# Kernel optimization log

Hardware: AMD Instinct MI355X
Metric: run time of the kernel (lower is better)

## Reference

```python
import jax, jax.numpy as jnp
import numpy as np

B, N, E = 128, 2048, 32768   # events, nodes per history graph, temporal edges per graph
C, TC, H = 4, 4, 2           # channels, time_channels, heads (hardcoded in source)
DH = C // H
L = 2                        # num_layers


def setup_inputs() -> dict:
    key = jax.random.key(0)
    ks = jax.random.split(key, 16)
    return {
        "x": jax.random.normal(ks[0], (B, N, C), jnp.float32),
        "edge_index": jax.random.randint(ks[1], (B, 2, E), 0, N),
        "edge_time": jax.random.uniform(ks[2], (B, E), jnp.float32),
        "timestamp": jax.random.uniform(ks[3], (B,), jnp.float32),
        "src_index": jax.random.randint(ks[4], (B,), 0, N),
        "dst_index": jax.random.randint(ks[5], (B,), 0, N),
        "time_w": jax.random.normal(ks[6], (TC,), jnp.float32),
        "time_b": jax.random.normal(ks[7], (TC,), jnp.float32),
        "Wq": jax.random.normal(ks[8], (L, C, C), jnp.float32) / np.sqrt(C).astype(np.float32),
        "Wk": jax.random.normal(ks[9], (L, C + TC, C), jnp.float32) / np.sqrt(C + TC).astype(np.float32),
        "Wv": jax.random.normal(ks[10], (L, C + TC, C), jnp.float32) / np.sqrt(C + TC).astype(np.float32),
        "Wo": jax.random.normal(ks[11], (L, C, C), jnp.float32) / np.sqrt(C).astype(np.float32),
        "bo": jnp.zeros((L, C), jnp.float32),
        "W_lin": jax.random.normal(ks[12], (2 * C + TC, 2), jnp.float32) / np.sqrt(2 * C + TC).astype(np.float32),
        "b_lin": jnp.zeros((2,), jnp.float32),
    }


def _time_enc(t, w, b):
    # TimeEncoder: cos(t * w + b)  (Bochner-style functional time encoding)
    return jnp.cos(t[..., None] * w + b)


def _encode(x, src, dst, phi, Wq, Wk, Wv, Wo, bo):
    # seg id per edge: (batch, dst node) -> flat segment for segment softmax
    seg = (jnp.arange(B, dtype=dst.dtype)[:, None] * N + dst).reshape(-1)  # [B*E]
    h = x
    for l in range(L):
        h_src = jnp.take_along_axis(h, src[:, :, None], axis=1)            # [B,E,C] gather source feats
        msg = jnp.concatenate([h_src, phi], axis=-1)                       # [B,E,C+TC]
        q = (h @ Wq[l]).reshape(B, N, C)                                   # [B,N,C]
        k = (msg @ Wk[l]).reshape(B, E, H, DH)
        v = (msg @ Wv[l]).reshape(B, E, H, DH)
        q_e = jnp.take_along_axis(q, dst[:, :, None], axis=1).reshape(B, E, H, DH)
        logits = (q_e * k).sum(-1) / np.float32(np.sqrt(DH))               # [B,E,H]
        lf = logits.reshape(B * E, H)
        m = jax.ops.segment_max(lf, seg, num_segments=B * N)               # stable softmax max
        p = jnp.exp(lf - m[seg])
        s = jax.ops.segment_sum(p, seg, num_segments=B * N)
        agg = jax.ops.segment_sum(p[:, :, None] * v.reshape(B * E, H, DH), seg, num_segments=B * N)
        attn = (agg / jnp.where(s == 0, 1.0, s)[:, :, None]).reshape(B, N, C)
        h = jax.nn.relu(h + attn @ Wo[l] + bo[l])                          # residual + out-proj + relu
    return h


def reference(x, edge_index, edge_time, timestamp, src_index, dst_index,
              time_w, time_b, Wq, Wk, Wv, Wo, bo, W_lin, b_lin):
    src, dst = edge_index[:, 0, :], edge_index[:, 1, :]
    dt = timestamp[:, None] - edge_time                                    # [B,E] time deltas vs query time
    phi = _time_enc(dt, time_w, time_b)                                    # [B,E,TC]
    h = _encode(x, src, dst, phi, Wq, Wk, Wv, Wo, bo)                      # [B,N,C]
    bidx = jnp.arange(B)
    src_x = h[bidx, src_index]                                             # [B,C]
    dst_x = h[bidx, dst_index]                                             # [B,C]
    time_x = _time_enc(timestamp, time_w, time_b)                          # [B,TC]
    feats = jnp.concatenate([src_x, dst_x, time_x], axis=-1)               # [B,12]
    return feats @ W_lin + b_lin                                           # [B,2]
```

## Files before the change

kernel.cpp:

```cpp
#include <hip/hip_runtime.h>

namespace {

constexpr int B = 128, N = 2048, E = 32768;
constexpr int LOG2N = 11, LOG2E = 15;
constexpr int QE = E / 4;
constexpr int LOG2QE = 13;

constexpr size_t OFF_H0 = 0;
constexpr size_t OFF_H1 = 4u * 1024 * 1024;
constexpr size_t OFF_S8 = 8u * 1024 * 1024;
constexpr size_t OFF_RP = 40u * 1024 * 1024;

__global__ __launch_bounds__(1024) void sort_kernel(const int* __restrict__ edge_index,
                                                    const float* __restrict__ edge_time,
                                                    const float* __restrict__ timestamp,
                                                    int2* __restrict__ sorted8,
                                                    int* __restrict__ row_ptr) {
  __shared__ int  cnt[N];
  __shared__ int  wsum[16];
  __shared__ int2 rec[QE];
  int blk = blockIdx.x, b = blk >> 2, q = blk & 3, t = threadIdx.x;

  cnt[t] = 0; cnt[t + 1024] = 0;
  __syncthreads();

  const int* src_arr = edge_index + (((size_t)(2 * b)) << LOG2E) + q * QE;
  const int* dst_arr = edge_index + (((size_t)(2 * b + 1)) << LOG2E) + q * QE;
  const float* et    = edge_time + (((size_t)b) << LOG2E) + q * QE;
  float ts = timestamp[b];

  for (int e = t; e < QE; e += 1024) atomicAdd(&cnt[dst_arr[e]], 1);
  __syncthreads();

  int i0 = 2 * t, i1 = 2 * t + 1;
  int l0 = cnt[i0], l1 = cnt[i1];
  int sum = l0 + l1;
  int lane = t & 63, wid = t >> 6;
  int incl = sum;
#pragma unroll
  for (int d = 1; d < 64; d <<= 1) {
    int v = __shfl_up(incl, d, 64);
    if (lane >= d) incl += v;
  }
  if (lane == 63) wsum[wid] = incl;
  __syncthreads();
  if (t < 16) {
    int v = wsum[t];
    int inc = v;
#pragma unroll
    for (int d = 1; d < 16; d <<= 1) {
      int u = __shfl_up(inc, d, 16);
      if (t >= d) inc += u;
    }
    wsum[t] = inc - v;
  }
  __syncthreads();
  int run = wsum[wid] + (incl - sum);
  int run2 = run + l0;
  int* rp = row_ptr + (size_t)blk * (N + 1);
  rp[i0] = run;
  rp[i1] = run2;
  if (t == 1023) rp[N] = QE;
  cnt[i0] = run;
  cnt[i1] = run2;
  __syncthreads();

  for (int e = t; e < QE; e += 1024) {
    int dst = dst_arr[e];
    int src = src_arr[e];
    float dt = ts - et[e];
    int pos = atomicAdd(&cnt[dst], 1);
    rec[pos] = make_int2(src, __float_as_int(dt));
  }
  __syncthreads();

  const int4* rec4 = (const int4*)rec;
  int4* out4 = (int4*)(sorted8 + (((size_t)blk) << LOG2QE));
#pragma unroll
  for (int i = t; i < QE / 2; i += 1024) out4[i] = rec4[i];
}

__global__ __launch_bounds__(1024) void layer_kernel(const float4* __restrict__ h_in,
                                                     float4* __restrict__ h_out,
                                                     const int* __restrict__ row_ptr,
                                                     const int2* __restrict__ sorted8,
                                                     const float* __restrict__ tw,
                                                     const float* __restrict__ tb,
                                                     const float* __restrict__ Wq,
                                                     const float* __restrict__ Wk,
                                                     const float* __restrict__ Wv,
                                                     const float* __restrict__ Wo,
                                                     const float* __restrict__ bo) {
  __shared__ float4 lh[N];
  int blk = blockIdx.x, b = blk >> 1, half = blk & 1, t = threadIdx.x;

  const float4* hb = h_in + (((size_t)b) << LOG2N);
  lh[t] = hb[t];
  lh[t + 1024] = hb[t + 1024];

  float twf[4], tbf[4], wq[16], wkh[16], wkp[16], wvh[16], wvp[16];
#pragma unroll
  for (int j = 0; j < 4; j++) { twf[j] = tw[j]; tbf[j] = tb[j]; }
#pragma unroll
  for (int j = 0; j < 16; j++) wq[j] = Wq[j];
#pragma unroll
  for (int j = 0; j < 16; j++) { wkh[j] = Wk[j]; wkp[j] = Wk[16 + j]; }
#pragma unroll
  for (int j = 0; j < 16; j++) { wvh[j] = Wv[j]; wvp[j] = Wv[16 + j]; }
  __syncthreads();

  int n = half * 1024 + t;
  float4 hn = lh[n];
  const float RS2 = 0.70710678118654752f;
  float q0 = (hn.x * wq[0] + hn.y * wq[4] + hn.z * wq[8]  + hn.w * wq[12]) * RS2;
  float q1 = (hn.x * wq[1] + hn.y * wq[5] + hn.z * wq[9]  + hn.w * wq[13]) * RS2;
  float q2 = (hn.x * wq[2] + hn.y * wq[6] + hn.z * wq[10] + hn.w * wq[14]) * RS2;
  float q3 = (hn.x * wq[3] + hn.y * wq[7] + hn.z * wq[11] + hn.w * wq[15]) * RS2;

  float wH0[4], wH1[4], wA[4], wB[4];
#pragma unroll
  for (int i = 0; i < 4; i++) {
    wH0[i] = q0 * wkh[i * 4 + 0] + q1 * wkh[i * 4 + 1];
    wH1[i] = q2 * wkh[i * 4 + 2] + q3 * wkh[i * 4 + 3];
    wA[i]  = q0 * wkp[i * 4 + 0] + q1 * wkp[i * 4 + 1];
    wB[i]  = q2 * wkp[i * 4 + 2] + q3 * wkp[i * 4 + 3];
  }

  int stage = 0;
  int addr, rem, total;
  int b1, b2, b3, c1, c2, c3;
  {
    const int* rp0 = row_ptr + (size_t)(b * 4 + 0) * (N + 1);
    const int* rp1 = row_ptr + (size_t)(b * 4 + 1) * (N + 1);
    const int* rp2 = row_ptr + (size_t)(b * 4 + 2) * (N + 1);
    const int* rp3 = row_ptr + (size_t)(b * 4 + 3) * (N + 1);
    int s0 = rp0[n], e0 = rp0[n + 1];
    int s1 = rp1[n], e1 = rp1[n + 1];
    int s2 = rp2[n], e2 = rp2[n + 1];
    int s3 = rp3[n], e3 = rp3[n + 1];
    int c0 = e0 - s0; c1 = e1 - s1; c2 = e2 - s2; c3 = e3 - s3;
    total = c0 + c1 + c2 + c3;
    addr = ((b * 4 + 0) << LOG2QE) + s0; rem = c0;
    b1 = ((b * 4 + 1) << LOG2QE) + s1;
    b2 = ((b * 4 + 2) << LOG2QE) + s2;
    b3 = ((b * 4 + 3) << LOG2QE) + s3;
  }
  while (rem == 0 && stage < 3) {
    ++stage;
    addr = (stage == 1) ? b1 : (stage == 2) ? b2 : b3;
    rem  = (stage == 1) ? c1 : (stage == 2) ? c2 : c3;
  }

  float m0 = -INFINITY, m1 = -INFINITY;
  float s0v = 0.f, s1v = 0.f, a00 = 0.f, a01 = 0.f, a10 = 0.f, a11 = 0.f;

  int2 rcCur = sorted8[addr];
  for (int it = 0; it < total; ++it) {
    int2 rc = rcCur;
    ++addr; --rem;
    while (rem == 0 && stage < 3) {
      ++stage;
      addr = (stage == 1) ? b1 : (stage == 2) ? b2 : b3;
      rem  = (stage == 1) ? c1 : (stage == 2) ? c2 : c3;
    }
    rcCur = sorted8[addr];

    float dt = __int_as_float(rc.y);
    float4 hs = lh[rc.x];
    float ph0 = __cosf(dt * twf[0] + tbf[0]);
    float ph1 = __cosf(dt * twf[1] + tbf[1]);
    float ph2 = __cosf(dt * twf[2] + tbf[2]);
    float ph3 = __cosf(dt * twf[3] + tbf[3]);

    float l0 = hs.x * wH0[0] + hs.y * wH0[1] + hs.z * wH0[2] + hs.w * wH0[3]
             + ph0 * wA[0] + ph1 * wA[1] + ph2 * wA[2] + ph3 * wA[3];
    float l1 = hs.x * wH1[0] + hs.y * wH1[1] + hs.z * wH1[2] + hs.w * wH1[3]
             + ph0 * wB[0] + ph1 * wB[1] + ph2 * wB[2] + ph3 * wB[3];

    float v0 = hs.x * wvh[0] + hs.y * wvh[4] + hs.z * wvh[8]  + hs.w * wvh[12]
             + ph0 * wvp[0] + ph1 * wvp[4] + ph2 * wvp[8]  + ph3 * wvp[12];
    float v1 = hs.x * wvh[1] + hs.y * wvh[5] + hs.z * wvh[9]  + hs.w * wvh[13]
             + ph0 * wvp[1] + ph1 * wvp[5] + ph2 * wvp[9]  + ph3 * wvp[13];
    float v2 = hs.x * wvh[2] + hs.y * wvh[6] + hs.z * wvh[10] + hs.w * wvh[14]
             + ph0 * wvp[2] + ph1 * wvp[6] + ph2 * wvp[10] + ph3 * wvp[14];
    float v3 = hs.x * wvh[3] + hs.y * wvh[7] + hs.z * wvh[11] + hs.w * wvh[15]
             + ph0 * wvp[3] + ph1 * wvp[7] + ph2 * wvp[11] + ph3 * wvp[15];

    float d0 = l0 - m0;
    float e0 = __expf(fminf(d0, -d0));
    bool  g0 = d0 > 0.f;
    float p0  = g0 ? 1.f : e0;
    float sc0 = g0 ? e0 : 1.f;
    m0 = fmaxf(m0, l0);
    s0v = s0v * sc0 + p0;
    a00 = a00 * sc0 + p0 * v0;
    a01 = a01 * sc0 + p0 * v1;
    float d1 = l1 - m1;
    float e1 = __expf(fminf(d1, -d1));
    bool  g1 = d1 > 0.f;
    float p1  = g1 ? 1.f : e1;
    float sc1 = g1 ? e1 : 1.f;
    m1 = fmaxf(m1, l1);
    s1v = s1v * sc1 + p1;
    a10 = a10 * sc1 + p1 * v2;
    a11 = a11 * sc1 + p1 * v3;
  }

  float den0 = (s0v == 0.f) ? 1.f : s0v;
  float den1 = (s1v == 0.f) ? 1.f : s1v;
  float at0 = a00 / den0, at1 = a01 / den0, at2 = a10 / den1, at3 = a11 / den1;

  float wof[16], bof[4];
#pragma unroll
  for (int j = 0; j < 16; j++) wof[j] = Wo[j];
#pragma unroll
  for (int j = 0; j < 4; j++) bof[j] = bo[j];

  float o0 = bof[0] + at0 * wof[0] + at1 * wof[4] + at2 * wof[8]  + at3 * wof[12];
  float o1 = bof[1] + at0 * wof[1] + at1 * wof[5] + at2 * wof[9]  + at3 * wof[13];
  float o2 = bof[2] + at0 * wof[2] + at1 * wof[6] + at2 * wof[10] + at3 * wof[14];
  float o3 = bof[3] + at0 * wof[3] + at1 * wof[7] + at2 * wof[11] + at3 * wof[15];
  h_out[(((size_t)b) << LOG2N) + n] =
      make_float4(fmaxf(hn.x + o0, 0.f), fmaxf(hn.y + o1, 0.f),
                  fmaxf(hn.z + o2, 0.f), fmaxf(hn.w + o3, 0.f));
}

__global__ void final_kernel(const float4* __restrict__ h,
                             const int* __restrict__ src_index, const int* __restrict__ dst_index,
                             const float* __restrict__ timestamp,
                             const float* __restrict__ tw,
                             const float* __restrict__ tb,
                             const float* __restrict__ W_lin,
                             const float* __restrict__ b_lin,
                             float* __restrict__ out) {
  int b = threadIdx.x;
  if (b >= B) return;
  float4 sx = h[(((size_t)b) << LOG2N) + src_index[b]];
  float4 dx = h[(((size_t)b) << LOG2N) + dst_index[b]];
  float ts = timestamp[b];
  float f[12];
  f[0] = sx.x; f[1] = sx.y; f[2] = sx.z; f[3] = sx.w;
  f[4] = dx.x; f[5] = dx.y; f[6] = dx.z; f[7] = dx.w;
#pragma unroll
  for (int j = 0; j < 4; j++) f[8 + j] = __cosf(ts * tw[j] + tb[j]);
#pragma unroll
  for (int c = 0; c < 2; c++) {
    float o = b_lin[c];
#pragma unroll
    for (int j = 0; j < 12; j++) o += f[j] * W_lin[j * 2 + c];
    out[b * 2 + c] = o;
  }
}

}

extern "C" void kernel_launch(void* const* d_in, const int* in_sizes, int n_in,
                              void* d_out, int out_size, void* d_ws, size_t ws_size,
                              hipStream_t stream) {
  (void)in_sizes; (void)n_in; (void)out_size; (void)ws_size;
  const float* x         = (const float*)d_in[0];
  const int*   edge_idx  = (const int*)d_in[1];
  const float* edge_time = (const float*)d_in[2];
  const float* timestamp = (const float*)d_in[3];
  const int*   src_index = (const int*)d_in[4];
  const int*   dst_index = (const int*)d_in[5];
  const float* time_w    = (const float*)d_in[6];
  const float* time_b    = (const float*)d_in[7];
  const float* Wq        = (const float*)d_in[8];
  const float* Wk        = (const float*)d_in[9];
  const float* Wv        = (const float*)d_in[10];
  const float* Wo        = (const float*)d_in[11];
  const float* bo        = (const float*)d_in[12];
  const float* W_lin     = (const float*)d_in[13];
  const float* b_lin     = (const float*)d_in[14];

  char* ws = (char*)d_ws;
  float4* h0      = (float4*)(ws + OFF_H0);
  float4* h1      = (float4*)(ws + OFF_H1);
  int2*   sorted8 = (int2*)(ws + OFF_S8);
  int*    row_ptr = (int*)(ws + OFF_RP);

  sort_kernel<<<4 * B, 1024, 0, stream>>>(edge_idx, edge_time, timestamp, sorted8, row_ptr);

  layer_kernel<<<2 * B, 1024, 0, stream>>>((const float4*)x, h1, row_ptr, sorted8,
                                           time_w, time_b,
                                           Wq + 0 * 16, Wk + 0 * 32, Wv + 0 * 32,
                                           Wo + 0 * 16, bo + 0 * 4);
  layer_kernel<<<2 * B, 1024, 0, stream>>>(h1, h0, row_ptr, sorted8,
                                           time_w, time_b,
                                           Wq + 1 * 16, Wk + 1 * 32, Wv + 1 * 32,
                                           Wo + 1 * 16, bo + 1 * 4);

  final_kernel<<<1, 128, 0, stream>>>(h0, src_index, dst_index, timestamp, time_w, time_b,
                                      W_lin, b_lin, (float*)d_out);
}
```

Before: 168.0 us.

## Drop online-softmax max tracking, use hardware cos/exp2, and process two edges per iteration

Removes the running-max rescaling from the per-node attention loop. Logits are pre-scaled by log2(e) so the loop can call v_exp_f32 directly, and each edge's weight simply adds into the sums. The time-encoding cos becomes a v_cos_f32 inline asm, with inputs pre-scaled by 1/(2π). The edge loop is unrolled by two with independent accumulators to break the serial dependency chain. Without max subtraction, exp can overflow for large logits, so correctness now depends on the logits staying small. The hardware cos may also lose accuracy for large arguments.

New measurement: 173.2 us. +3.1%, slower.

```diff
diff --git a/kernel.cpp b/kernel.cpp
--- a/kernel.cpp
+++ b/kernel.cpp
@@ -99,9 +99,11 @@
   lh[t] = hb[t];
   lh[t + 1024] = hb[t + 1024];
 
-  float twf[4], tbf[4], wq[16], wkh[16], wkp[16], wvh[16], wvp[16];
-#pragma unroll
-  for (int j = 0; j < 4; j++) { twf[j] = tw[j]; tbf[j] = tb[j]; }
+  constexpr float INV2PI = 0.15915494309189535f;
+  constexpr float QSCALE = 0.70710678118654752f * 1.4426950408889634f;
+  float twf2[4], tbf2[4], wq[16], wkh[16], wkp[16], wvh[16], wvp[16];
+#pragma unroll
+  for (int j = 0; j < 4; j++) { twf2[j] = tw[j] * INV2PI; tbf2[j] = tb[j] * INV2PI; }
 #pragma unroll
   for (int j = 0; j < 16; j++) wq[j] = Wq[j];
 #pragma unroll
@@ -111,24 +113,22 @@
   __syncthreads();
 
   int n = half * 1024 + t;
-  float4 hn = lh[n];
-  const float RS2 = 0.70710678118654752f;
-  float q0 = (hn.x * wq[0] + hn.y * wq[4] + hn.z * wq[8]  + hn.w * wq[12]) * RS2;
-  float q1 = (hn.x * wq[1] + hn.y * wq[5] + hn.z * wq[9]  + hn.w * wq[13]) * RS2;
-  float q2 = (hn.x * wq[2] + hn.y * wq[6] + hn.z * wq[10] + hn.w * wq[14]) * RS2;
-  float q3 = (hn.x * wq[3] + hn.y * wq[7] + hn.z * wq[11] + hn.w * wq[15]) * RS2;
-
-  float wH0[4], wH1[4], wA[4], wB[4];
-#pragma unroll
-  for (int i = 0; i < 4; i++) {
-    wH0[i] = q0 * wkh[i * 4 + 0] + q1 * wkh[i * 4 + 1];
-    wH1[i] = q2 * wkh[i * 4 + 2] + q3 * wkh[i * 4 + 3];
-    wA[i]  = q0 * wkp[i * 4 + 0] + q1 * wkp[i * 4 + 1];
-    wB[i]  = q2 * wkp[i * 4 + 2] + q3 * wkp[i * 4 + 3];
-  }
-
-  int stage = 0;
-  int addr, rem, total;
+  {
+    float4 hn = lh[n];
+    float q0 = (hn.x * wq[0] + hn.y * wq[4] + hn.z * wq[8]  + hn.w * wq[12]) * QSCALE;
+    float q1 = (hn.x * wq[1] + hn.y * wq[5] + hn.z * wq[9]  + hn.w * wq[13]) * QSCALE;
+    float q2 = (hn.x * wq[2] + hn.y * wq[6] + hn.z * wq[10] + hn.w * wq[14]) * QSCALE;
+    float q3 = (hn.x * wq[3] + hn.y * wq[7] + hn.z * wq[11] + hn.w * wq[15]) * QSCALE;
+#pragma unroll
+    for (int i = 0; i < 4; i++) {
+      wq[i]      = q0 * wkh[i * 4 + 0] + q1 * wkh[i * 4 + 1];
+      wq[4 + i]  = q2 * wkh[i * 4 + 2] + q3 * wkh[i * 4 + 3];
+      wq[8 + i]  = q0 * wkp[i * 4 + 0] + q1 * wkp[i * 4 + 1];
+      wq[12 + i] = q2 * wkp[i * 4 + 2] + q3 * wkp[i * 4 + 3];
+    }
+  }
+
+  int stage = 0, addr, rem, total;
   int b1, b2, b3, c1, c2, c3;
   {
     const int* rp0 = row_ptr + (size_t)(b * 4 + 0) * (N + 1);
@@ -145,67 +145,94 @@
     b1 = ((b * 4 + 1) << LOG2QE) + s1;
     b2 = ((b * 4 + 2) << LOG2QE) + s2;
     b3 = ((b * 4 + 3) << LOG2QE) + s3;
-  }
-  while (rem == 0 && stage < 3) {
-    ++stage;
-    addr = (stage == 1) ? b1 : (stage == 2) ? b2 : b3;
-    rem  = (stage == 1) ? c1 : (stage == 2) ? c2 : c3;
-  }
-
-  float m0 = -INFINITY, m1 = -INFINITY;
-  float s0v = 0.f, s1v = 0.f, a00 = 0.f, a01 = 0.f, a10 = 0.f, a11 = 0.f;
-
-  int2 rcCur = sorted8[addr];
-  for (int it = 0; it < total; ++it) {
-    int2 rc = rcCur;
-    ++addr; --rem;
-    while (rem == 0 && stage < 3) {
+    while (rem <= 0 && stage < 3) {
       ++stage;
       addr = (stage == 1) ? b1 : (stage == 2) ? b2 : b3;
       rem  = (stage == 1) ? c1 : (stage == 2) ? c2 : c3;
     }
-    rcCur = sorted8[addr];
-
-    float dt = __int_as_float(rc.y);
-    float4 hs = lh[rc.x];
-    float ph0 = __cosf(dt * twf[0] + tbf[0]);
-    float ph1 = __cosf(dt * twf[1] + tbf[1]);
-    float ph2 = __cosf(dt * twf[2] + tbf[2]);
-    float ph3 = __cosf(dt * twf[3] + tbf[3]);
-
-    float l0 = hs.x * wH0[0] + hs.y * wH0[1] + hs.z * wH0[2] + hs.w * wH0[3]
-             + ph0 * wA[0] + ph1 * wA[1] + ph2 * wA[2] + ph3 * wA[3];
-    float l1 = hs.x * wH1[0] + hs.y * wH1[1] + hs.z * wH1[2] + hs.w * wH1[3]
-             + ph0 * wB[0] + ph1 * wB[1] + ph2 * wB[2] + ph3 * wB[3];
-
-    float v0 = hs.x * wvh[0] + hs.y * wvh[4] + hs.z * wvh[8]  + hs.w * wvh[12]
-             + ph0 * wvp[0] + ph1 * wvp[4] + ph2 * wvp[8]  + ph3 * wvp[12];
-    float v1 = hs.x * wvh[1] + hs.y * wvh[5] + hs.z * wvh[9]  + hs.w * wvh[13]
-             + ph0 * wvp[1] + ph1 * wvp[5] + ph2 * wvp[9]  + ph3 * wvp[13];
-    float v2 = hs.x * wvh[2] + hs.y * wvh[6] + hs.z * wvh[10] + hs.w * wvh[14]
-             + ph0 * wvp[2] + ph1 * wvp[6] + ph2 * wvp[10] + ph3 * wvp[14];
-    float v3 = hs.x * wvh[3] + hs.y * wvh[7] + hs.z * wvh[11] + hs.w * wvh[15]
-             + ph0 * wvp[3] + ph1 * wvp[7] + ph2 * wvp[11] + ph3 * wvp[15];
-
-    float d0 = l0 - m0;
-    float e0 = __expf(fminf(d0, -d0));
-    bool  g0 = d0 > 0.f;
-    float p0  = g0 ? 1.f : e0;
-    float sc0 = g0 ? e0 : 1.f;
-    m0 = fmaxf(m0, l0);
-    s0v = s0v * sc0 + p0;
-    a00 = a00 * sc0 + p0 * v0;
-    a01 = a01 * sc0 + p0 * v1;
-    float d1 = l1 - m1;
-    float e1 = __expf(fminf(d1, -d1));
-    bool  g1 = d1 > 0.f;
-    float p1  = g1 ? 1.f : e1;
-    float sc1 = g1 ? e1 : 1.f;
-    m1 = fmaxf(m1, l1);
-    s1v = s1v * sc1 + p1;
-    a10 = a10 * sc1 + p1 * v2;
-    a11 = a11 * sc1 + p1 * v3;
-  }
+  }
+
+#define ADV() do { ++addr; --rem;                                   \
+    while (rem <= 0 && stage < 3) { ++stage;                        \
+      addr = (stage == 1) ? b1 : (stage == 2) ? b2 : b3;            \
+      rem  = (stage == 1) ? c1 : (stage == 2) ? c2 : c3; } } while (0)
+#define HW_COS(d, s) asm("v_cos_f32 %0, %1" : "=v"(d) : "v"(s))
+#define HW_EXP2(d, s) asm("v_exp_f32 %0, %1" : "=v"(d) : "v"(s))
+
+  float sA0 = 0.f, sA1 = 0.f, aA00 = 0.f, aA01 = 0.f, aA10 = 0.f, aA11 = 0.f;
+  float sB0 = 0.f, sB1 = 0.f, aB00 = 0.f, aB01 = 0.f, aB10 = 0.f, aB11 = 0.f;
+
+  int itc = (total + 1) >> 1;
+  int2 rA = sorted8[addr]; ADV();
+  int2 rB = sorted8[addr]; ADV();
+
+  for (int it = 0; it < itc; ++it) {
+    int2 cA = rA, cB = rB;
+    rA = sorted8[addr]; ADV();
+    rB = sorted8[addr]; ADV();
+
+    bool vB = (2 * it + 1) < total;
+    float dtA = __int_as_float(cA.y);
+    float dtB = vB ? __int_as_float(cB.y) : 0.f;
+    float4 hsA = lh[cA.x & (N - 1)];
+    float4 hsB = lh[cB.x & (N - 1)];
+
+    float phA0, phA1, phA2, phA3, phB0, phB1, phB2, phB3;
+    HW_COS(phA0, dtA * twf2[0] + tbf2[0]);
+    HW_COS(phA1, dtA * twf2[1] + tbf2[1]);
+    HW_COS(phA2, dtA * twf2[2] + tbf2[2]);
+    HW_COS(phA3, dtA * twf2[3] + tbf2[3]);
+    HW_COS(phB0, dtB * twf2[0] + tbf2[0]);
+    HW_COS(phB1, dtB * twf2[1] + tbf2[1]);
+    HW_COS(phB2, dtB * twf2[2] + tbf2[2]);
+    HW_COS(phB3, dtB * twf2[3] + tbf2[3]);
+
+    float lA0 = hsA.x * wq[0] + hsA.y * wq[1] + hsA.z * wq[2]  + hsA.w * wq[3]
+              + phA0 * wq[8] + phA1 * wq[9] + phA2 * wq[10] + phA3 * wq[11];
+    float lA1 = hsA.x * wq[4] + hsA.y * wq[5] + hsA.z * wq[6]  + hsA.w * wq[7]
+              + phA0 * wq[12] + phA1 * wq[13] + phA2 * wq[14] + phA3 * wq[15];
+    float lB0 = hsB.x * wq[0] + hsB.y * wq[1] + hsB.z * wq[2]  + hsB.w * wq[3]
+              + phB0 * wq[8] + phB1 * wq[9] + phB2 * wq[10] + phB3 * wq[11];
+    float lB1 = hsB.x * wq[4] + hsB.y * wq[5] + hsB.z * wq[6]  + hsB.w * wq[7]
+              + phB0 * wq[12] + phB1 * wq[13] + phB2 * wq[14] + phB3 * wq[15];
+
+    float pA0, pA1, eB0, eB1;
+    HW_EXP2(pA0, lA0);
+    HW_EXP2(pA1, lA1);
+    HW_EXP2(eB0, lB0);
+    HW_EXP2(eB1, lB1);
+    float pB0 = vB ? eB0 : 0.f;
+    float pB1 = vB ? eB1 : 0.f;
+
+    float vA0 = hsA.x * wvh[0] + hsA.y * wvh[4] + hsA.z * wvh[8]  + hsA.w * wvh[12]
+              + phA0 * wvp[0] + phA1 * wvp[4] + phA2 * wvp[8]  + phA3 * wvp[12];
+    float vA1 = hsA.x * wvh[1] + hsA.y * wvh[5] + hsA.z * wvh[9]  + hsA.w * wvh[13]
+              + phA0 * wvp[1] + phA1 * wvp[5] + phA2 * wvp[9]  + phA3 * wvp[13];
+    float vA2 = hsA.x * wvh[2] + hsA.y * wvh[6] + hsA.z * wvh[10] + hsA.w * wvh[14]
+              + phA0 * wvp[2] + phA1 * wvp[6] + phA2 * wvp[10] + phA3 * wvp[14];
+    float vA3 = hsA.x * wvh[3] + hsA.y * wvh[7] + hsA.z * wvh[11] + hsA.w * wvh[15]
+              + phA0 * wvp[3] + phA1 * wvp[7] + phA2 * wvp[11] + phA3 * wvp[15];
+    float vB0 = hsB.x * wvh[0] + hsB.y * wvh[4] + hsB.z * wvh[8]  + hsB.w * wvh[12]
+              + phB0 * wvp[0] + phB1 * wvp[4] + phB2 * wvp[8]  + phB3 * wvp[12];
+    float vB1 = hsB.x * wvh[1] + hsB.y * wvh[5] + hsB.z * wvh[9]  + hsB.w * wvh[13]
+              + phB0 * wvp[1] + phB1 * wvp[5] + phB2 * wvp[9]  + phB3 * wvp[13];
+    float vB2 = hsB.x * wvh[2] + hsB.y * wvh[6] + hsB.z * wvh[10] + hsB.w * wvh[14]
+              + phB0 * wvp[2] + phB1 * wvp[6] + phB2 * wvp[10] + phB3 * wvp[14];
+    float vB3 = hsB.x * wvh[3] + hsB.y * wvh[7] + hsB.z * wvh[11] + hsB.w * wvh[15]
+              + phB0 * wvp[3] + phB1 * wvp[7] + phB2 * wvp[11] + phB3 * wvp[15];
+
+    sA0 += pA0; aA00 += pA0 * vA0; aA01 += pA0 * vA1;
+    sA1 += pA1; aA10 += pA1 * vA2; aA11 += pA1 * vA3;
+    sB0 += pB0; aB00 += pB0 * vB0; aB01 += pB0 * vB1;
+    sB1 += pB1; aB10 += pB1 * vB2; aB11 += pB1 * vB3;
+  }
+#undef ADV
+#undef HW_COS
+#undef HW_EXP2
+
+  float s0v = sA0 + sB0, s1v = sA1 + sB1;
+  float a00 = aA00 + aB00, a01 = aA01 + aB01;
+  float a10 = aA10 + aB10, a11 = aA11 + aB11;
 
   float den0 = (s0v == 0.f) ? 1.f : s0v;
   float den1 = (s1v == 0.f) ? 1.f : s1v;
@@ -217,6 +244,7 @@
 #pragma unroll
   for (int j = 0; j < 4; j++) bof[j] = bo[j];
 
+  float4 hn = lh[n];
   float o0 = bof[0] + at0 * wof[0] + at1 * wof[4] + at2 * wof[8]  + at3 * wof[12];
   float o1 = bof[1] + at0 * wof[1] + at1 * wof[5] + at2 * wof[9]  + at3 * wof[13];
   float o2 = bof[2] + at0 * wof[2] + at1 * wof[6] + at2 * wof[10] + at3 * wof[14];
```
